# Performance work log

Hardware: AMD Instinct MI355X
Metric: run time of the kernel (lower is better)

Reference implementation:

```python
import jax, jax.numpy as jnp
import numpy as np

H = 12          # num_heads
T = 8           # num_temp_tokens (frames per video clip)


def _conv1d(z, w, b):
    # z: (Bv, C, T), w: (C_out, C_in, 3), padding=1, stride=1 (matches nn.Conv1d)
    y = jax.lax.conv_general_dilated(z, w, window_strides=(1,), padding=[(1, 1)],
                                     dimension_numbers=('NCH', 'OIH', 'NCH'))
    return y + b[None, :, None]


def setup_inputs() -> dict:
    key = jax.random.key(0)
    ks = jax.random.split(key, 9)
    B, N, C = 64, 197, 768
    s = 0.02
    return {
        'x': jax.random.normal(ks[0], (B, N, C), jnp.float32),
        'w_qkv': jax.random.normal(ks[1], (3 * C, C), jnp.float32) * s,
        'b_qkv': jax.random.normal(ks[2], (3 * C,), jnp.float32) * s,
        'w_proj': jax.random.normal(ks[3], (C, C), jnp.float32) * s,
        'b_proj': jax.random.normal(ks[4], (C,), jnp.float32) * s,
        'conv_q_w': jax.random.normal(ks[5], (C, C, 3), jnp.float32) * s,
        'conv_q_b': jax.random.normal(ks[6], (C,), jnp.float32) * s,
        'conv_k_w': jax.random.normal(ks[7], (C, C, 3), jnp.float32) * s,
        'conv_k_b': jax.random.normal(ks[8], (C,), jnp.float32) * s,
    }


def reference(x, w_qkv, b_qkv, w_proj, b_proj, conv_q_w, conv_q_b, conv_k_w, conv_k_b):
    B, N, C = x.shape
    Dh = C // H
    scale = Dh ** -0.5

    # temporal context from the CLS token across frames of each clip
    g = x[:, 0, :].reshape(B // T, T, C).transpose(0, 2, 1)          # (Bv, C, T)
    tcq = _conv1d(g, conv_q_w, conv_q_b).transpose(0, 2, 1).reshape(B, H, 1, Dh)
    tck = _conv1d(g, conv_k_w, conv_k_b).transpose(0, 2, 1).reshape(B, H, 1, Dh)

    qkv = (x @ w_qkv.T + b_qkv).reshape(B, N, 3, H, Dh).transpose(2, 0, 3, 1, 4)
    q, k, v = qkv[0], qkv[1], qkv[2]                                  # (B, H, N, Dh)

    # bias-added attention: (q + tcq) (k + tck)^T
    scores = jnp.einsum('bhnd,bhmd->bhnm', q + tcq, k + tck) * scale  # (B, H, N, N)
    attn = jax.nn.softmax(scores, axis=-1)
    out = jnp.einsum('bhnm,bhmd->bhnd', attn, v)                      # (B, H, N, Dh)
    out = out.transpose(0, 2, 1, 3).reshape(B, N, C)
    return out @ w_proj.T + b_proj
```

## Files before the change

### kernel.cpp

```cpp
#include <hip/hip_runtime.h>
#include <hip/hip_bf16.h>
#include <stdint.h>

typedef __attribute__((ext_vector_type(8))) short s16x8;
typedef __attribute__((ext_vector_type(4))) float f32x4;

#define MFMA16(a, b, c) __builtin_amdgcn_mfma_f32_16x16x32_bf16((a), (b), (c), 0, 0, 0)
#define SBAR() __builtin_amdgcn_s_barrier()

__device__ __forceinline__ void gl_lds16(const void* g, void* l) {
  __builtin_amdgcn_global_load_lds(
      (__attribute__((address_space(1))) void*)(void*)g,
      (__attribute__((address_space(3))) void*)l,
      16, 0, 0);
}

__device__ __forceinline__ unsigned short f2bf(float f) {
  union { float f; uint32_t u; } c; c.f = f;
  return (unsigned short)((c.u + 0x7FFFu + ((c.u >> 16) & 1u)) >> 16);
}

__device__ __forceinline__ f32x4 max4(f32x4 a, f32x4 b) {
  f32x4 c;
  c[0] = fmaxf(a[0], b[0]); c[1] = fmaxf(a[1], b[1]);
  c[2] = fmaxf(a[2], b[2]); c[3] = fmaxf(a[3], b[3]);
  return c;
}

__device__ __forceinline__ void xcd_swz(int GX, int GY, int& bx, int& by) {
  int nwg = GX * GY;
  int lid = by * GX + bx;
  int q = nwg >> 3, rm = nwg & 7;
  int xcd = lid & 7, off = lid >> 3;
  int nid = (xcd < rm ? xcd * (q + 1) : rm * (q + 1) + (xcd - rm) * q) + off;
  bx = nid % GX;
  by = nid / GX;
}

__global__ __launch_bounds__(256) void cvt_all(
    const float* __restrict__ a, unsigned short* __restrict__ oa, int na4,
    const float* __restrict__ b, unsigned short* __restrict__ ob, int nb4,
    const float* __restrict__ c, unsigned short* __restrict__ oc, int nc4) {
  int i = blockIdx.x * 256 + threadIdx.x;
  const float* src; unsigned short* dst; int j;
  if (i < na4) { src = a; dst = oa; j = i; }
  else if (i < na4 + nb4) { src = b; dst = ob; j = i - na4; }
  else if (i < na4 + nb4 + nc4) { src = c; dst = oc; j = i - na4 - nb4; }
  else return;
  float4 v = ((const float4*)src)[j];
  ushort4 o;
  o.x = f2bf(v.x); o.y = f2bf(v.y); o.z = f2bf(v.z); o.w = f2bf(v.w);
  ((ushort4*)dst)[j] = o;
}

__global__ __launch_bounds__(256) void conv_cls(
    const float* __restrict__ x,
    const float* __restrict__ wq, const float* __restrict__ bq,
    const float* __restrict__ wk, const float* __restrict__ bk,
    float* __restrict__ tcq, float* __restrict__ tck) {
  __shared__ float g[768][10];
  const int tid = threadIdx.x;
  const int clip = blockIdx.y;
  const int chunk = blockIdx.x;
  for (int i = tid; i < 768 * 8; i += 256) {
    int tt = i / 768, ci = i % 768;
    g[ci][tt + 1] = x[(size_t)(clip * 8 + tt) * 151296 + ci];
  }
  for (int i = tid; i < 768; i += 256) { g[i][0] = 0.f; g[i][9] = 0.f; }
  __syncthreads();
  const int co = chunk * 32 + (tid >> 3);
  const int t = tid & 7;
  float aq = 0.f, ak = 0.f;
  const float* wqp = wq + (size_t)co * 2304;
  const float* wkp = wk + (size_t)co * 2304;
  for (int ci = 0; ci < 768; ++ci) {
    float g0 = g[ci][t], g1 = g[ci][t + 1], g2 = g[ci][t + 2];
    aq += g0 * wqp[ci * 3 + 0] + g1 * wqp[ci * 3 + 1] + g2 * wqp[ci * 3 + 2];
    ak += g0 * wkp[ci * 3 + 0] + g1 * wkp[ci * 3 + 1] + g2 * wkp[ci * 3 + 2];
  }
  int b = clip * 8 + t;
  tcq[b * 768 + co] = aq + bq[co];
  tck[b * 768 + co] = ak + bk[co];
}

__global__ __launch_bounds__(1024, 4) void qkv_attn(
    const unsigned short* __restrict__ X,
    const unsigned short* __restrict__ Wq,
    const float* __restrict__ bias,
    const float* __restrict__ tcq, const float* __restrict__ tck,
    unsigned short* __restrict__ O) {
  union __align__(16) Smem {
    struct {
      unsigned short Xs[3][208][64];
      unsigned short Ws[3][192][64];
    } st;
    struct {
      unsigned short Qs[208][72];
      unsigned short Ks[208][72];
      unsigned short VTs[64][232];
      unsigned short Ps[13][16][40];
    } at;
  };
  __shared__ Smem U;
  __shared__ float tcb[3][64];

  const int tid = threadIdx.x;
  const int w = tid >> 6, lane = tid & 63;
  int bx = blockIdx.x, by0 = 0;
  xcd_swz(gridDim.x, 1, bx, by0);
  const int b = bx / 12, h = bx % 12;

  if (tid < 192) {
    int sec = tid >> 6, d = tid & 63;
    float v = bias[sec * 768 + h * 64 + d];
    if (sec == 0) v += tcq[b * 768 + h * 64 + d];
    else if (sec == 1) v += tck[b * 768 + h * 64 + d];
    tcb[sec][d] = v;
  }

  const int wm = w >> 2, wn = w & 3;
  const int r = lane & 15, gq = lane >> 4;
  const int lrow = lane >> 3;
  const int lsw = ((lane & 7) ^ (lrow & 7)) * 8;
  const int mfn = (wm == 3) ? 4 : 3;

  f32x4 acc[4][3] = {};
  const size_t xbase = (size_t)b * 197 * 768;

  auto stage = [&](int buf, int kc) {
#pragma unroll
    for (int j = 0; j < 2; ++j) {
      int c = w + j * 16;
      if (c < 26) {
        int row = c * 8 + lrow;
        gl_lds16(X + xbase + (size_t)row * 768 + kc * 64 + lsw,
                 (char*)&U.st.Xs[buf][0][0] + c * 1024);
      }
    }
#pragma unroll
    for (int j = 0; j < 2; ++j) {
      int c = w + j * 16;
      if (c < 24) {
        int wrow = c * 8 + lrow;
        int sec = wrow >> 6;
        gl_lds16(Wq + (size_t)(sec * 768 + h * 64 + (wrow & 63)) * 768 + kc * 64 + lsw,
                 (char*)&U.st.Ws[buf][0][0] + c * 1024);
      }
    }
  };

#define WAIT_OWN()                                                 \
  do {                                                             \
    if (w < 8)       asm volatile("s_waitcnt vmcnt(4)" ::: "memory"); \
    else if (w < 10) asm volatile("s_waitcnt vmcnt(3)" ::: "memory"); \
    else             asm volatile("s_waitcnt vmcnt(2)" ::: "memory"); \
  } while (0)

  stage(0, 0);
  stage(1, 1);
  WAIT_OWN();
  SBAR();

  for (int kc = 0; kc < 12; ++kc) {
    const int cb = kc % 3;
    if (kc + 2 < 12) stage((kc + 2) % 3, kc + 2);
    const char* xb = (const char*)&U.st.Xs[cb][0][0];
    const char* wb = (const char*)&U.st.Ws[cb][0][0];
    __builtin_amdgcn_s_setprio(1);
#pragma unroll
    for (int kk = 0; kk < 2; ++kk) {
      s16x8 bfrg[3];
#pragma unroll
      for (int nf = 0; nf < 3; ++nf) {
        int row = wn * 48 + nf * 16 + r;
        bfrg[nf] = *(const s16x8*)(wb + row * 128 + (((kk * 4 + gq) ^ (r & 7)) * 16));
      }
#pragma unroll
      for (int mf = 0; mf < 4; ++mf) {
        if (mf < mfn) {
          int row = wm * 48 + mf * 16 + r;
          s16x8 afr = *(const s16x8*)(xb + row * 128 + (((kk * 4 + gq) ^ (r & 7)) * 16));
#pragma unroll
          for (int nf = 0; nf < 3; ++nf) acc[mf][nf] = MFMA16(afr, bfrg[nf], acc[mf][nf]);
        }
      }
    }
    __builtin_amdgcn_s_setprio(0);
    if (kc < 10) {
      WAIT_OWN();
      SBAR();
    } else if (kc == 10) {
      asm volatile("s_waitcnt vmcnt(0)" ::: "memory");
      SBAR();
    }
  }
  __syncthreads();

  for (int i = tid; i < 64 * 35; i += 1024) {
    int d = i / 35, c = 197 + i % 35;
    U.at.VTs[d][c] = 0;
  }
#pragma unroll
  for (int mf = 0; mf < 4; ++mf) {
    if (mf < mfn) {
#pragma unroll
      for (int nf = 0; nf < 3; ++nf) {
        int ncol = wn * 48 + nf * 16 + r;
        int sec = ncol >> 6, d = ncol & 63;
        float bb = tcb[sec][d];
#pragma unroll
        for (int rr = 0; rr < 4; ++rr) {
          int mrow = wm * 48 + mf * 16 + gq * 4 + rr;
          unsigned short bv = f2bf(acc[mf][nf][rr] + bb);
          if (sec == 0)      U.at.Qs[mrow][d] = bv;
          else if (sec == 1) U.at.Ks[mrow][d] = bv;
          else if (mrow < 197) U.at.VTs[d][mrow] = bv;
        }
      }
    }
  }
  __syncthreads();

  const int g = gq;
  for (int qt = w; qt < 13; qt += 16) {
    const int q0 = qt * 16;
    int qrow = q0 + r; if (qrow > 196) qrow = 196;
    s16x8 aq0 = *(const s16x8*)&U.at.Qs[qrow][g * 8];
    s16x8 aq1 = *(const s16x8*)&U.at.Qs[qrow][32 + g * 8];

    f32x4 s[13];
    __builtin_amdgcn_s_setprio(1);
#pragma unroll
    for (int j = 0; j < 13; ++j) {
      f32x4 z = {};
      z = MFMA16(aq0, *(const s16x8*)&U.at.Ks[j * 16 + r][g * 8], z);
      z = MFMA16(aq1, *(const s16x8*)&U.at.Ks[j * 16 + r][32 + g * 8], z);
      s[j] = z;
    }
    __builtin_amdgcn_s_setprio(0);
    if (r >= 5) { s[12][0] = -1e30f; s[12][1] = -1e30f; s[12][2] = -1e30f; s[12][3] = -1e30f; }

    f32x4 mx = s[0];
#pragma unroll
    for (int j = 1; j < 13; ++j) mx = max4(mx, s[j]);
#pragma unroll
    for (int off = 1; off < 16; off <<= 1) {
      f32x4 o_;
      o_[0] = __shfl_xor(mx[0], off, 64); o_[1] = __shfl_xor(mx[1], off, 64);
      o_[2] = __shfl_xor(mx[2], off, 64); o_[3] = __shfl_xor(mx[3], off, 64);
      mx = max4(mx, o_);
    }
    const float cexp = 0.125f * 1.44269504088896f;
    f32x4 sum = {};
#pragma unroll
    for (int j = 0; j < 13; ++j) {
      f32x4 p;
      p[0] = exp2f((s[j][0] - mx[0]) * cexp); p[1] = exp2f((s[j][1] - mx[1]) * cexp);
      p[2] = exp2f((s[j][2] - mx[2]) * cexp); p[3] = exp2f((s[j][3] - mx[3]) * cexp);
      s[j] = p;
      sum += p;
    }
#pragma unroll
    for (int off = 1; off < 16; off <<= 1) {
      sum[0] += __shfl_xor(sum[0], off, 64); sum[1] += __shfl_xor(sum[1], off, 64);
      sum[2] += __shfl_xor(sum[2], off, 64); sum[3] += __shfl_xor(sum[3], off, 64);
    }

    f32x4 o4[4] = {};
    for (int ks = 0; ks < 7; ++ks) {
      int j0 = ks * 2;
#pragma unroll
      for (int jj = 0; jj < 2; ++jj) {
        int jt = j0 + jj;
        int colb = jj * 16 + r;
        if (jt < 13) {
          f32x4 p = s[jt < 13 ? jt : 0];
          U.at.Ps[w][g * 4 + 0][colb] = f2bf(p[0]);
          U.at.Ps[w][g * 4 + 1][colb] = f2bf(p[1]);
          U.at.Ps[w][g * 4 + 2][colb] = f2bf(p[2]);
          U.at.Ps[w][g * 4 + 3][colb] = f2bf(p[3]);
        } else {
          U.at.Ps[w][g * 4 + 0][colb] = 0; U.at.Ps[w][g * 4 + 1][colb] = 0;
          U.at.Ps[w][g * 4 + 2][colb] = 0; U.at.Ps[w][g * 4 + 3][colb] = 0;
        }
      }
      asm volatile("s_waitcnt lgkmcnt(0)" ::: "memory");
      s16x8 ap = *(const s16x8*)&U.at.Ps[w][r][g * 8];
      __builtin_amdgcn_s_setprio(1);
#pragma unroll
      for (int n = 0; n < 4; ++n)
        o4[n] = MFMA16(ap, *(const s16x8*)&U.at.VTs[n * 16 + r][ks * 32 + g * 8], o4[n]);
      __builtin_amdgcn_s_setprio(0);
    }

    f32x4 rinv;
    rinv[0] = 1.0f / sum[0]; rinv[1] = 1.0f / sum[1];
    rinv[2] = 1.0f / sum[2]; rinv[3] = 1.0f / sum[3];
#pragma unroll
    for (int n = 0; n < 4; ++n) {
#pragma unroll
      for (int rr = 0; rr < 4; ++rr) {
        int qr = q0 + g * 4 + rr;
        if (qr < 197)
          O[((size_t)(b * 197 + qr)) * 768 + h * 64 + n * 16 + r] = f2bf(o4[n][rr] * rinv[rr]);
      }
    }
  }
#undef WAIT_OWN
}

__global__ __launch_bounds__(512, 4) void proj_gemm(
    const unsigned short* __restrict__ A,
    const unsigned short* __restrict__ Bw,
    const float* __restrict__ bias,
    float* __restrict__ Out) {
  __shared__ __align__(16) unsigned short As[2][192][64];
  __shared__ __align__(16) unsigned short Bs[2][128][64];
  const int tid = threadIdx.x;
  const int w = tid >> 6, lane = tid & 63;
  const int wm = w >> 1, wn = w & 1;
  const int r = lane & 15, gq = lane >> 4;
  int bx = blockIdx.x, by = blockIdx.y;
  xcd_swz(gridDim.x, gridDim.y, bx, by);
  const int m0 = by * 192, n0 = bx * 128;
  const int lrow = lane >> 3;
  const int lsw = ((lane & 7) ^ (lrow & 7)) * 8;

  f32x4 acc[3][4] = {};

  auto stage = [&](int buf, int kt) {
#pragma unroll
    for (int j = 0; j < 3; ++j) {
      int c = w + j * 8;
      int row = c * 8 + lrow;
      gl_lds16(A + (size_t)(m0 + row) * 768 + kt * 64 + lsw, (char*)&As[buf][0][0] + c * 1024);
    }
#pragma unroll
    for (int j = 0; j < 2; ++j) {
      int c = w + j * 8;
      int row = c * 8 + lrow;
      gl_lds16(Bw + (size_t)(n0 + row) * 768 + kt * 64 + lsw, (char*)&Bs[buf][0][0] + c * 1024);
    }
  };

  stage(0, 0);
  stage(1, 1);
  asm volatile("s_waitcnt vmcnt(5)" ::: "memory");
  SBAR();

  for (int kt = 0; kt < 12; ++kt) {
    const int cur = kt & 1;
    s16x8 af[2][3], bfr[2][4];
#pragma unroll
    for (int kk = 0; kk < 2; ++kk) {
#pragma unroll
      for (int m = 0; m < 3; ++m) {
        int row = wm * 48 + m * 16 + r;
        af[kk][m] = *(const s16x8*)((const char*)&As[cur][0][0] + row * 128 +
                                    (((kk * 4 + gq) ^ (r & 7)) * 16));
      }
#pragma unroll
      for (int n = 0; n < 4; ++n) {
        int row = wn * 64 + n * 16 + r;
        bfr[kk][n] = *(const s16x8*)((const char*)&Bs[cur][0][0] + row * 128 +
                                     (((kk * 4 + gq) ^ (r & 7)) * 16));
      }
    }
    asm volatile("s_waitcnt lgkmcnt(0)" ::: "memory");
    __builtin_amdgcn_sched_barrier(0);
    SBAR();
    if (kt + 2 < 12) stage(cur, kt + 2);
    __builtin_amdgcn_s_setprio(1);
#pragma unroll
    for (int kk = 0; kk < 2; ++kk)
#pragma unroll
      for (int m = 0; m < 3; ++m)
#pragma unroll
        for (int n = 0; n < 4; ++n) acc[m][n] = MFMA16(af[kk][m], bfr[kk][n], acc[m][n]);
    __builtin_amdgcn_s_setprio(0);
    if (kt < 11) {
      if (kt < 10) asm volatile("s_waitcnt vmcnt(5)" ::: "memory");
      else         asm volatile("s_waitcnt vmcnt(0)" ::: "memory");
      SBAR();
    }
  }

#pragma unroll
  for (int m = 0; m < 3; ++m) {
#pragma unroll
    for (int n = 0; n < 4; ++n) {
#pragma unroll
      for (int rr = 0; rr < 4; ++rr) {
        int M = m0 + wm * 48 + m * 16 + gq * 4 + rr;
        int N = n0 + wn * 64 + n * 16 + r;
        if (M < 12608) Out[(size_t)M * 768 + N] = acc[m][n][rr] + bias[N];
      }
    }
  }
}

extern "C" void kernel_launch(void* const* d_in, const int* in_sizes, int n_in,
                              void* d_out, int out_size, void* d_ws, size_t ws_size,
                              hipStream_t stream) {
  const float* x       = (const float*)d_in[0];
  const float* w_qkv   = (const float*)d_in[1];
  const float* b_qkv   = (const float*)d_in[2];
  const float* w_proj  = (const float*)d_in[3];
  const float* b_proj  = (const float*)d_in[4];
  const float* conv_qw = (const float*)d_in[5];
  const float* conv_qb = (const float*)d_in[6];
  const float* conv_kw = (const float*)d_in[7];
  const float* conv_kb = (const float*)d_in[8];
  float* out = (float*)d_out;

  char* ws = (char*)d_ws;
  size_t off = 0;
  auto alloc = [&](size_t n) {
    char* p = ws + off;
    off = (off + n + 255) & ~(size_t)255;
    return p;
  };
  unsigned short* x_bf    = (unsigned short*)alloc(12608ull * 768 * 2);
  unsigned short* ao_bf   = (unsigned short*)alloc(12608ull * 768 * 2);
  unsigned short* wqkv_bf = (unsigned short*)alloc(2304ull * 768 * 2);
  unsigned short* wproj_bf= (unsigned short*)alloc(768ull * 768 * 2);
  float* tcq = (float*)alloc(64 * 768 * 4);
  float* tck = (float*)alloc(64 * 768 * 4);
  if (off > ws_size) return;

  const int na4 = 2420736, nb4 = 442368, nc4 = 147456;
  cvt_all<<<dim3((na4 + nb4 + nc4 + 255) / 256), 256, 0, stream>>>(
      x, x_bf, na4, w_qkv, wqkv_bf, nb4, w_proj, wproj_bf, nc4);
  conv_cls<<<dim3(24, 8), 256, 0, stream>>>(x, conv_qw, conv_qb, conv_kw, conv_kb, tcq, tck);
  qkv_attn<<<dim3(768), 1024, 0, stream>>>(x_bf, wqkv_bf, b_qkv, tcq, tck, ao_bf);
  proj_gemm<<<dim3(6, 66), 512, 0, stream>>>(ao_bf, wproj_bf, b_proj, out);
}
```

Measured before the change: 187.4 us.

## Transpose QK^T MFMA so each lane owns a query row, packing P as bf16 pairs

Swaps the MFMA operands of the score computation so each lane's accumulator holds keys for a single query row. The row max and sum now need only two cross-group shuffles instead of four-step butterflies on four values. Probabilities are packed to bf16 in registers and written to LDS as 8-byte stores in a new blocked layout, in two halves, rather than as scalar 16-bit stores. This cuts LDS traffic and waitcnt stalls inside the PV loop, at the cost of more complex slot indexing and a shuffle to redistribute row sums at the end.

```diff
diff --git a/kernel.cpp b/kernel.cpp
--- a/kernel.cpp
+++ b/kernel.cpp
@@ -18,13 +18,6 @@
 __device__ __forceinline__ unsigned short f2bf(float f) {
   union { float f; uint32_t u; } c; c.f = f;
   return (unsigned short)((c.u + 0x7FFFu + ((c.u >> 16) & 1u)) >> 16);
-}
-
-__device__ __forceinline__ f32x4 max4(f32x4 a, f32x4 b) {
-  f32x4 c;
-  c[0] = fmaxf(a[0], b[0]); c[1] = fmaxf(a[1], b[1]);
-  c[2] = fmaxf(a[2], b[2]); c[3] = fmaxf(a[3], b[3]);
-  return c;
 }
 
 __device__ __forceinline__ void xcd_swz(int GX, int GY, int& bx, int& by) {
@@ -98,7 +91,7 @@
       unsigned short Qs[208][72];
       unsigned short Ks[208][72];
       unsigned short VTs[64][232];
-      unsigned short Ps[13][16][40];
+      uint32_t Pb[13][7][16][4][2];
     } at;
   };
   __shared__ Smem U;
@@ -225,67 +218,69 @@
   for (int qt = w; qt < 13; qt += 16) {
     const int q0 = qt * 16;
     int qrow = q0 + r; if (qrow > 196) qrow = 196;
-    s16x8 aq0 = *(const s16x8*)&U.at.Qs[qrow][g * 8];
-    s16x8 aq1 = *(const s16x8*)&U.at.Qs[qrow][32 + g * 8];
+    s16x8 bq0 = *(const s16x8*)&U.at.Qs[qrow][g * 8];
+    s16x8 bq1 = *(const s16x8*)&U.at.Qs[qrow][32 + g * 8];
 
     f32x4 s[13];
     __builtin_amdgcn_s_setprio(1);
 #pragma unroll
     for (int j = 0; j < 13; ++j) {
       f32x4 z = {};
-      z = MFMA16(aq0, *(const s16x8*)&U.at.Ks[j * 16 + r][g * 8], z);
-      z = MFMA16(aq1, *(const s16x8*)&U.at.Ks[j * 16 + r][32 + g * 8], z);
+      z = MFMA16(*(const s16x8*)&U.at.Ks[j * 16 + r][g * 8], bq0, z);
+      z = MFMA16(*(const s16x8*)&U.at.Ks[j * 16 + r][32 + g * 8], bq1, z);
       s[j] = z;
     }
     __builtin_amdgcn_s_setprio(0);
-    if (r >= 5) { s[12][0] = -1e30f; s[12][1] = -1e30f; s[12][2] = -1e30f; s[12][3] = -1e30f; }
-
-    f32x4 mx = s[0];
-#pragma unroll
-    for (int j = 1; j < 13; ++j) mx = max4(mx, s[j]);
-#pragma unroll
-    for (int off = 1; off < 16; off <<= 1) {
-      f32x4 o_;
-      o_[0] = __shfl_xor(mx[0], off, 64); o_[1] = __shfl_xor(mx[1], off, 64);
-      o_[2] = __shfl_xor(mx[2], off, 64); o_[3] = __shfl_xor(mx[3], off, 64);
-      mx = max4(mx, o_);
-    }
+    if (g >= 2) { s[12][0] = -1e30f; s[12][1] = -1e30f; s[12][2] = -1e30f; s[12][3] = -1e30f; }
+    else if (g == 1) { s[12][1] = -1e30f; s[12][2] = -1e30f; s[12][3] = -1e30f; }
+
+    float mx = s[0][0];
+#pragma unroll
+    for (int j = 0; j < 13; ++j)
+      mx = fmaxf(mx, fmaxf(fmaxf(s[j][0], s[j][1]), fmaxf(s[j][2], s[j][3])));
+    mx = fmaxf(mx, __shfl_xor(mx, 16, 64));
+    mx = fmaxf(mx, __shfl_xor(mx, 32, 64));
+
     const float cexp = 0.125f * 1.44269504088896f;
-    f32x4 sum = {};
+    float sum = 0.f;
+    uint32_t pw[13][2];
 #pragma unroll
     for (int j = 0; j < 13; ++j) {
-      f32x4 p;
-      p[0] = exp2f((s[j][0] - mx[0]) * cexp); p[1] = exp2f((s[j][1] - mx[1]) * cexp);
-      p[2] = exp2f((s[j][2] - mx[2]) * cexp); p[3] = exp2f((s[j][3] - mx[3]) * cexp);
-      s[j] = p;
-      sum += p;
-    }
-#pragma unroll
-    for (int off = 1; off < 16; off <<= 1) {
-      sum[0] += __shfl_xor(sum[0], off, 64); sum[1] += __shfl_xor(sum[1], off, 64);
-      sum[2] += __shfl_xor(sum[2], off, 64); sum[3] += __shfl_xor(sum[3], off, 64);
-    }
+      float p0 = exp2f((s[j][0] - mx) * cexp);
+      float p1 = exp2f((s[j][1] - mx) * cexp);
+      float p2 = exp2f((s[j][2] - mx) * cexp);
+      float p3 = exp2f((s[j][3] - mx) * cexp);
+      sum += (p0 + p1) + (p2 + p3);
+      pw[j][0] = ((uint32_t)f2bf(p1) << 16) | f2bf(p0);
+      pw[j][1] = ((uint32_t)f2bf(p3) << 16) | f2bf(p2);
+    }
+    sum += __shfl_xor(sum, 16, 64);
+    sum += __shfl_xor(sum, 32, 64);
+
+#pragma unroll
+    for (int j = 0; j < 7; ++j) {
+      uint2 v; v.x = pw[j][0]; v.y = pw[j][1];
+      *(uint2*)&U.at.Pb[w][j][r][g][0] = v;
+    }
+    asm volatile("s_waitcnt lgkmcnt(0)" ::: "memory");
 
     f32x4 o4[4] = {};
+    s16x8 zero8 = {};
+#pragma unroll
     for (int ks = 0; ks < 7; ++ks) {
-      int j0 = ks * 2;
-#pragma unroll
-      for (int jj = 0; jj < 2; ++jj) {
-        int jt = j0 + jj;
-        int colb = jj * 16 + r;
-        if (jt < 13) {
-          f32x4 p = s[jt < 13 ? jt : 0];
-          U.at.Ps[w][g * 4 + 0][colb] = f2bf(p[0]);
-          U.at.Ps[w][g * 4 + 1][colb] = f2bf(p[1]);
-          U.at.Ps[w][g * 4 + 2][colb] = f2bf(p[2]);
-          U.at.Ps[w][g * 4 + 3][colb] = f2bf(p[3]);
-        } else {
-          U.at.Ps[w][g * 4 + 0][colb] = 0; U.at.Ps[w][g * 4 + 1][colb] = 0;
-          U.at.Ps[w][g * 4 + 2][colb] = 0; U.at.Ps[w][g * 4 + 3][colb] = 0;
+      if (ks == 3) {
+#pragma unroll
+        for (int j = 7; j < 13; ++j) {
+          uint2 v; v.x = pw[j][0]; v.y = pw[j][1];
+          *(uint2*)&U.at.Pb[w][j - 7][r][g][0] = v;
         }
-      }
-      asm volatile("s_waitcnt lgkmcnt(0)" ::: "memory");
-      s16x8 ap = *(const s16x8*)&U.at.Ps[w][r][g * 8];
+        asm volatile("s_waitcnt lgkmcnt(0)" ::: "memory");
+      }
+      const int slotA = (2 * ks) % 7, slotB = (2 * ks + 1) % 7;
+      const uint32_t* pa = (g & 2) ? &U.at.Pb[w][slotB][r][2 * (g & 1)][0]
+                                   : &U.at.Pb[w][slotA][r][2 * (g & 1)][0];
+      s16x8 ap = *(const s16x8*)pa;
+      if (ks == 6 && (g & 2)) ap = zero8;
       __builtin_amdgcn_s_setprio(1);
 #pragma unroll
       for (int n = 0; n < 4; ++n)
@@ -293,9 +288,9 @@
       __builtin_amdgcn_s_setprio(0);
     }
 
-    f32x4 rinv;
-    rinv[0] = 1.0f / sum[0]; rinv[1] = 1.0f / sum[1];
-    rinv[2] = 1.0f / sum[2]; rinv[3] = 1.0f / sum[3];
+    float rinv[4];
+#pragma unroll
+    for (int rr = 0; rr < 4; ++rr) rinv[rr] = 1.0f / __shfl(sum, g * 4 + rr, 64);
 #pragma unroll
     for (int n = 0; n < 4; ++n) {
 #pragma unroll
```

Result: no change. 188.3 us (+0.5%).
